# Kernel optimization log

Hardware: AMD Instinct MI355X
Metric: run time of the kernel (lower is better)

## Reference

```python
import jax, jax.numpy as jnp
import numpy as np

B, T, DIM, H, E, D, K = 2, 2048, 1024, 8, 5, 64, 3


def setup_inputs() -> dict:
    key = jax.random.key(0)
    ks = jax.random.split(key, 7)
    s = 0.02
    return {
        "x": jax.random.normal(ks[0], (B, T, DIM), dtype=jnp.float32),
        "w_q": jax.random.normal(ks[1], (DIM, H * E * D), dtype=jnp.float32) * s,
        "w_kv": jax.random.normal(ks[2], (DIM, 2 * H * E * D), dtype=jnp.float32) * s,
        "w_s": jax.random.normal(ks[3], (DIM, H * E), dtype=jnp.float32) * s,
        "w_d": jax.random.normal(ks[4], (DIM, H * E), dtype=jnp.float32) * s,
        "w_o_w": jax.random.normal(ks[5], (H, DIM, D), dtype=jnp.float32) * s,
        "w_o_b": jax.random.normal(ks[6], (H, DIM), dtype=jnp.float32) * s,
    }


def _select(proj_full, eps, s):
    # Faithful to torch scatter_(3, eps, s): value s[..., k] is written at
    # expert slot eps[..., k]; multiplying the full projection by that sparse
    # score tensor and summing over e == gather selected experts, weight by
    # the FIRST K raw scores (not the topk values), and sum.
    sel = jnp.take_along_axis(proj_full, eps[..., None], axis=3)  # b t h K d
    return (sel * s[..., :K, None]).sum(axis=3)  # b t h d


def reference(x, w_q, w_kv, w_s, w_d, w_o_w, w_o_b):
    scale = D ** (-0.5)
    ss = jax.nn.sigmoid(x @ w_s).reshape(B, T, H, E)
    sd = jax.nn.sigmoid(x @ w_d).reshape(B, T, H, E)
    eps_s = jax.lax.top_k(ss, K)[1]  # b t h K
    eps_d = jax.lax.top_k(sd, K)[1]

    q_full = (x @ w_q).reshape(B, T, H, E, D)
    q = _select(q_full, eps_d, sd)  # b t h d

    kv_full = (x @ w_kv).reshape(B, T, 2, H, E, D)
    k = _select(kv_full[:, :, 0], eps_s, ss)
    v = _select(kv_full[:, :, 1], eps_s, ss)

    attn = jnp.einsum("bihd,bjhd->bhij", q * scale, k)
    probs = jax.nn.softmax(attn, axis=-1)
    out = jnp.einsum("bhij,bjhd->bihd", probs, v)  # b t h d

    # per-head Linear(dim_head, dim) then sum over heads (stack+sum)
    return jnp.einsum("bihd,hfd->bif", out, w_o_w) + w_o_b.sum(axis=0)
```

## Files before the change

### kernel.cpp

```cpp
#include <hip/hip_runtime.h>

#define DEV __device__ __forceinline__

typedef float f32x4 __attribute__((ext_vector_type(4)));
typedef short s16x8 __attribute__((ext_vector_type(8)));
typedef unsigned short u16;
typedef unsigned int u32;

constexpr int Bb = 2, Tt = 2048, DIMc = 1024, Hh = 8, Ee = 5, Dd = 64;
constexpr int NTOK = Bb * Tt;
constexpr int NQ = Hh * Ee * Dd;

DEV u16 f2bf(float f) {
  union { float f; u32 u; } v; v.f = f;
  u32 r = v.u + 0x7fffu + ((v.u >> 16) & 1u);
  return (u16)(r >> 16);
}

DEV u32 pk2(float a, float b) {
  return (u32)f2bf(a) | ((u32)f2bf(b) << 16);
}

DEV s16x8 ld8(const u16* p) {
  uint4 u = *reinterpret_cast<const uint4*>(p);
  return __builtin_bit_cast(s16x8, u);
}

DEV f32x4 mfma16(s16x8 a, s16x8 b, f32x4 c) {
  return __builtin_amdgcn_mfma_f32_16x16x32_bf16(a, b, c, 0, 0, 0);
}

DEV void gld16(const void* g, void* l) {
  __builtin_amdgcn_global_load_lds(
      (const __attribute__((address_space(1))) void*)g,
      (__attribute__((address_space(3))) void*)l, 16, 0, 0);
}


__global__ void k_cvt_x(const float* __restrict__ x, u16* __restrict__ xb) {
  int i = blockIdx.x * blockDim.x + threadIdx.x;
  float4 v = reinterpret_cast<const float4*>(x)[i];
  u16 r0 = f2bf(v.x), r1 = f2bf(v.y), r2 = f2bf(v.z), r3 = f2bf(v.w);
  u32 lo = (u32)r0 | ((u32)r1 << 16);
  u32 hi = (u32)r2 | ((u32)r3 << 16);
  reinterpret_cast<uint2*>(xb)[i] = make_uint2(lo, hi);
}

__global__ void k_tr_w(const float* __restrict__ wq, const float* __restrict__ wkv,
                       u16* __restrict__ wT) {
  int R0 = blockIdx.x * 32;
  int C0 = blockIdx.y * 32;
  int s = R0 / 2560, rem = R0 % 2560;
  int h = rem / 320, n0 = rem % 320;
  const float* src; int ld; int col0;
  if (s == 0) { src = wq;  ld = 2560; col0 = h * 320 + n0; }
  else        { src = wkv; ld = 5120; col0 = (s - 1) * 2560 + h * 320 + n0; }
  __shared__ float tile[32][33];
  int tx = threadIdx.x, ty = threadIdx.y;
  #pragma unroll
  for (int i = 0; i < 4; i++) {
    int c = C0 + ty + 8 * i;
    tile[ty + 8 * i][tx] = src[(size_t)c * ld + col0 + tx];
  }
  __syncthreads();
  #pragma unroll
  for (int i = 0; i < 4; i++) {
    int n = ty + 8 * i;
    wT[(size_t)(R0 + n) * 1024 + C0 + tx] = f2bf(tile[tx][n]);
  }
}

__global__ void k_tr_wo(const float* __restrict__ wow, u16* __restrict__ woT) {
  int f = blockIdx.x, d = threadIdx.x;
  #pragma unroll
  for (int h = 0; h < 8; h++)
    woT[(size_t)f * 512 + h * 64 + d] = f2bf(wow[((size_t)h * 1024 + f) * 64 + d]);
}

__global__ void k_bias(const float* __restrict__ wob, float* __restrict__ biasum) {
  int f = blockIdx.x * 256 + threadIdx.x;
  float s = 0.f;
  #pragma unroll
  for (int h = 0; h < 8; h++) s += wob[h * 1024 + f];
  biasum[f] = s;
}

__global__ void k_tr_wsd(const float* __restrict__ ws, const float* __restrict__ wd,
                         float* __restrict__ wsdT) {
  int j = blockIdx.x;
  const float* src = (j < 40) ? ws : wd;
  int c = (j < 40) ? j : j - 40;
  for (int i = threadIdx.x; i < 1024; i += 256)
    wsdT[(size_t)j * 1024 + i] = src[(size_t)i * 40 + c];
}

__launch_bounds__(320)
__global__ void k_scores(const float* __restrict__ x, const float* __restrict__ wsdT,
                         int* __restrict__ eps_s, int* __restrict__ eps_d,
                         float* __restrict__ ss3, float* __restrict__ sd3) {
  int tokb = blockIdx.x * 8;
  __shared__ float xl[8][1028];
  __shared__ float sc[8][80];
  const float4* xsrc = reinterpret_cast<const float4*>(x + (size_t)tokb * 1024);
  for (int i = threadIdx.x; i < 2048; i += 320) {
    int tok = i >> 8, col4 = i & 255;
    *reinterpret_cast<float4*>(&xl[tok][col4 * 4]) = xsrc[i];
  }
  __syncthreads();
  {
    int tok = threadIdx.x & 7, j = threadIdx.x >> 3;
    const float4* wsp = reinterpret_cast<const float4*>(wsdT + (size_t)j * 1024);
    const float4* wdp = reinterpret_cast<const float4*>(wsdT + (size_t)(j + 40) * 1024);
    float as0 = 0.f, as1 = 0.f, ad0 = 0.f, ad1 = 0.f;
    #pragma unroll 4
    for (int k4 = 0; k4 < 256; k4 += 2) {
      float4 x0 = *reinterpret_cast<const float4*>(&xl[tok][k4 * 4]);
      float4 x1 = *reinterpret_cast<const float4*>(&xl[tok][k4 * 4 + 4]);
      float4 wsv0 = wsp[k4], wsv1 = wsp[k4 + 1];
      float4 wdv0 = wdp[k4], wdv1 = wdp[k4 + 1];
      as0 += x0.x * wsv0.x + x0.y * wsv0.y + x0.z * wsv0.z + x0.w * wsv0.w;
      as1 += x1.x * wsv1.x + x1.y * wsv1.y + x1.z * wsv1.z + x1.w * wsv1.w;
      ad0 += x0.x * wdv0.x + x0.y * wdv0.y + x0.z * wdv0.z + x0.w * wdv0.w;
      ad1 += x1.x * wdv1.x + x1.y * wdv1.y + x1.z * wdv1.z + x1.w * wdv1.w;
    }
    float as = as0 + as1, ad = ad0 + ad1;
    sc[tok][j]      = 1.f / (1.f + expf(-as));
    sc[tok][40 + j] = 1.f / (1.f + expf(-ad));
  }
  __syncthreads();
  int t2 = threadIdx.x;
  if (t2 < 128) {
    int tt = t2 >> 4, u = t2 & 15, h = u >> 1, which = u & 1;
    const float* S = &sc[tt][which * 40 + h * 5];
    float v[5];
    #pragma unroll
    for (int e = 0; e < 5; e++) v[e] = S[e];
    int tok = tokb + tt;
    int base = (tok * 8 + h) * 3;
    int* eps = which ? eps_d : eps_s;
    float* w3 = which ? sd3 : ss3;
    bool used[5] = {false, false, false, false, false};
    #pragma unroll
    for (int kk = 0; kk < 3; kk++) {
      float best = -1e30f; int bi = 0;
      #pragma unroll
      for (int e = 0; e < 5; e++)
        if (!used[e] && v[e] > best) { best = v[e]; bi = e; }
      used[bi] = true;
      eps[base + kk] = bi;
    }
    #pragma unroll
    for (int kk = 0; kk < 3; kk++) w3[base + kk] = S[kk];
  }
}

__launch_bounds__(512)
__global__ void k_proj(const u16* __restrict__ xb, const u16* __restrict__ wT,
                       const int* __restrict__ eps_d, const int* __restrict__ eps_s,
                       const float* __restrict__ sd3, const float* __restrict__ ss3,
                       u16* __restrict__ qw, u16* __restrict__ kw, u16* __restrict__ vw) {
  int tok0 = blockIdx.x * 128;
  int h = blockIdx.y;
  int s = blockIdx.z;
  int Rbase = (s * 8 + h) * 320;
  __shared__ alignas(16) u16 bsA[128 * 64];
  __shared__ alignas(16) u16 bsB[320 * 64];
  int wv = threadIdx.x >> 6, l = threadIdx.x & 63;
  int g = l >> 4, c = l & 15;
  f32x4 acc[20];
  #pragma unroll
  for (int i = 0; i < 20; i++) acc[i] = (f32x4){0.f, 0.f, 0.f, 0.f};

  const u16* wTp0 = wT + (size_t)Rbase * 1024;
  const u16* xbp0 = xb + (size_t)tok0 * 1024;

  for (int k0 = 0; k0 < 1024; k0 += 64) {
    __syncthreads();
    const u16* wTp = wTp0 + k0;
    #pragma unroll
    for (int j = 0; j < 5; j++) {
      int ch = wv * 320 + j * 64 + l;
      int row = ch >> 3, part = ch & 7;
      gld16(wTp + (size_t)row * 1024 + ((part * 8) ^ ((row & 7) * 8)),
            &bsB[(wv * 320 + j * 64) * 8]);
    }
    const u16* xbp = xbp0 + k0;
    #pragma unroll
    for (int j = 0; j < 2; j++) {
      int ch = wv * 128 + j * 64 + l;
      int row = ch >> 3, part = ch & 7;
      gld16(xbp + (size_t)row * 1024 + ((part * 8) ^ ((row & 7) * 8)),
            &bsA[(wv * 128 + j * 64) * 8]);
    }
    __syncthreads();

    #pragma unroll
    for (int kk = 0; kk < 2; kk++) {
      int off = (kk * 32 + g * 8) ^ ((c & 7) * 8);
      s16x8 a = *reinterpret_cast<const s16x8*>(&bsA[(wv * 16 + c) * 64 + off]);
      #pragma unroll
      for (int nt = 0; nt < 20; nt++) {
        s16x8 b = *reinterpret_cast<const s16x8*>(&bsB[(nt * 16 + c) * 64 + off]);
        acc[nt] = mfma16(a, b, acc[nt]);
      }
    }
  }

  const int* eps = (s == 0) ? eps_d : eps_s;
  const float* w3 = (s == 0) ? sd3 : ss3;
  float scale = (s == 0) ? 0.125f : 1.0f;
  u16* dst = (s == 0) ? qw : (s == 1 ? kw : vw);
  #pragma unroll
  for (int r = 0; r < 4; r++) {
    int tokr = tok0 + wv * 16 + g * 4 + r;
    int base = (tokr * 8 + h) * 3;
    int e0 = eps[base], e1 = eps[base + 1], e2 = eps[base + 2];
    float w0 = w3[base], w1 = w3[base + 1], w2 = w3[base + 2];
    float we[5];
    #pragma unroll
    for (int e = 0; e < 5; e++)
      we[e] = (e0 == e ? w0 : 0.f) + (e1 == e ? w1 : 0.f) + (e2 == e ? w2 : 0.f);
    int b = tokr >> 11, t = tokr & 2047;
    size_t obase = (((size_t)b * 8 + h) * 2048 + t) * 64;
    #pragma unroll
    for (int dh = 0; dh < 4; dh++) {
      float vq = 0.f;
      #pragma unroll
      for (int e = 0; e < 5; e++) vq += we[e] * acc[e * 4 + dh][r];
      dst[obase + dh * 16 + c] = f2bf(vq * scale);
    }
  }
}

__global__ void k_trv(const u16* __restrict__ vw, u16* __restrict__ vT) {
  int bh = blockIdx.z;
  int t0 = blockIdx.x * 32, d0 = blockIdx.y * 32;
  __shared__ u16 tile[32][33];
  const u16* src = vw + (size_t)bh * 2048 * 64;
  u16* dst = vT + (size_t)bh * 64 * 2048;
  int tx = threadIdx.x, ty = threadIdx.y;
  #pragma unroll
  for (int i = 0; i < 4; i++)
    tile[ty + 8 * i][tx] = src[(size_t)(t0 + ty + 8 * i) * 64 + d0 + tx];
  __syncthreads();
  int p = 8 * ((tx & 15) >> 2) + (tx & 3) + ((tx >= 16) ? 4 : 0);
  #pragma unroll
  for (int i = 0; i < 4; i++)
    dst[(size_t)(d0 + ty + 8 * i) * 2048 + t0 + p] = tile[tx][ty + 8 * i];
}

__launch_bounds__(256)
__global__ void k_attn(const u16* __restrict__ qw, const u16* __restrict__ kw,
                       const u16* __restrict__ vT, u16* __restrict__ ow) {
  int bh = blockIdx.y;
  int b = bh >> 3, h = bh & 7;
  int q0 = blockIdx.x * 64;
  int wv = threadIdx.x >> 6, l = threadIdx.x & 63;
  int g = l >> 4, c = l & 15;
  const u16* qp = qw + (size_t)bh * 2048 * 64;
  const u16* kp = kw + (size_t)bh * 2048 * 64;
  const u16* vp = vT + (size_t)bh * 64 * 2048;
  __shared__ alignas(16) u16 Kl[128 * 64];
  __shared__ alignas(16) u16 Vl[64 * 128];

  s16x8 qa0 = ld8(qp + (size_t)(q0 + wv * 16 + c) * 64 + 0 + 8 * g);
  s16x8 qa1 = ld8(qp + (size_t)(q0 + wv * 16 + c) * 64 + 32 + 8 * g);

  f32x4 o[4];
  #pragma unroll
  for (int i = 0; i < 4; i++) o[i] = (f32x4){0.f, 0.f, 0.f, 0.f};
  float ssum = 0.f;

  for (int kt = 0; kt < 2048; kt += 128) {
    __syncthreads();
    #pragma unroll
    for (int j = 0; j < 4; j++) {
      int ch = (wv * 4 + j) * 64 + l;
      int row = ch >> 3, sl = ch & 7;
      gld16(kp + (size_t)(kt + row) * 64 + ((sl ^ (row & 7)) * 8),
            &Kl[(wv * 4 + j) * 64 * 8]);
    }
    #pragma unroll
    for (int j = 0; j < 4; j++) {
      int ch = (wv * 4 + j) * 64 + l;
      int d = ch >> 4, sl = ch & 15;
      gld16(vp + (size_t)d * 2048 + kt + ((sl ^ (d & 15)) * 8),
            &Vl[(wv * 4 + j) * 64 * 8]);
    }
    __syncthreads();

    #pragma unroll
    for (int kk = 0; kk < 4; kk++) {
      int r0 = kk * 32 + c, r1 = kk * 32 + 16 + c;
      int c7 = c & 7;
      s16x8 ka0 = *reinterpret_cast<const s16x8*>(&Kl[r0 * 64 + ((0 + g) ^ c7) * 8]);
      s16x8 ka1 = *reinterpret_cast<const s16x8*>(&Kl[r0 * 64 + ((4 + g) ^ c7) * 8]);
      s16x8 kc0 = *reinterpret_cast<const s16x8*>(&Kl[r1 * 64 + ((0 + g) ^ c7) * 8]);
      s16x8 kc1 = *reinterpret_cast<const s16x8*>(&Kl[r1 * 64 + ((4 + g) ^ c7) * 8]);

      f32x4 s0 = (f32x4){0.f, 0.f, 0.f, 0.f};
      f32x4 s1 = (f32x4){0.f, 0.f, 0.f, 0.f};
      s0 = mfma16(ka0, qa0, s0);
      s0 = mfma16(ka1, qa1, s0);
      s1 = mfma16(kc0, qa0, s1);
      s1 = mfma16(kc1, qa1, s1);

      float p00 = __expf(s0[0]), p01 = __expf(s0[1]);
      float p02 = __expf(s0[2]), p03 = __expf(s0[3]);
      float p10 = __expf(s1[0]), p11 = __expf(s1[1]);
      float p12 = __expf(s1[2]), p13 = __expf(s1[3]);
      ssum += (p00 + p01) + (p02 + p03) + (p10 + p11) + (p12 + p13);

      uint4 pw = make_uint4(pk2(p00, p01), pk2(p02, p03),
                            pk2(p10, p11), pk2(p12, p13));
      s16x8 pa = __builtin_bit_cast(s16x8, pw);

      #pragma unroll
      for (int nt = 0; nt < 4; nt++) {
        int d = nt * 16 + c;
        s16x8 vb = *reinterpret_cast<const s16x8*>(&Vl[d * 128 + (((kk * 4 + g) ^ (d & 15)) * 8)]);
        o[nt] = mfma16(pa, vb, o[nt]);
      }
    }
  }

  ssum += __shfl_xor(ssum, 16, 64);
  ssum += __shfl_xor(ssum, 32, 64);
  #pragma unroll
  for (int r = 0; r < 4; r++) {
    float sm = __shfl(ssum, g * 4 + r, 64);
    float inv = 1.f / sm;
    int t = q0 + wv * 16 + g * 4 + r;
    #pragma unroll
    for (int nt = 0; nt < 4; nt++)
      ow[((size_t)(b * 2048 + t)) * 512 + h * 64 + nt * 16 + c] = f2bf(o[nt][r] * inv);
  }
}

__launch_bounds__(512)
__global__ void k_oproj(const u16* __restrict__ ow, const u16* __restrict__ woT,
                        const float* __restrict__ biasum, float* __restrict__ out) {
  int t0 = blockIdx.x * 128, f0 = blockIdx.y * 64;
  int wv = threadIdx.x >> 6, l = threadIdx.x & 63;
  int g = l >> 4, c = l & 15;
  f32x4 acc[4];
  #pragma unroll
  for (int i = 0; i < 4; i++) acc[i] = (f32x4){0.f, 0.f, 0.f, 0.f};
  for (int k0 = 0; k0 < 512; k0 += 32) {
    s16x8 a = ld8(ow + (size_t)(t0 + wv * 16 + c) * 512 + k0 + 8 * g);
    #pragma unroll
    for (int nt = 0; nt < 4; nt++) {
      s16x8 bfr = ld8(woT + (size_t)(f0 + nt * 16 + c) * 512 + k0 + 8 * g);
      acc[nt] = mfma16(a, bfr, acc[nt]);
    }
  }
  #pragma unroll
  for (int r = 0; r < 4; r++) {
    int t = t0 + wv * 16 + g * 4 + r;
    #pragma unroll
    for (int nt = 0; nt < 4; nt++) {
      int f = f0 + nt * 16 + c;
      out[(size_t)t * 1024 + f] = acc[nt][r] + biasum[f];
    }
  }
}

extern "C" void kernel_launch(void* const* d_in, const int* in_sizes, int n_in,
                              void* d_out, int out_size, void* d_ws, size_t ws_size,
                              hipStream_t stream) {
  const float* x    = (const float*)d_in[0];
  const float* w_q  = (const float*)d_in[1];
  const float* w_kv = (const float*)d_in[2];
  const float* w_s  = (const float*)d_in[3];
  const float* w_d  = (const float*)d_in[4];
  const float* w_ow = (const float*)d_in[5];
  const float* w_ob = (const float*)d_in[6];
  float* out = (float*)d_out;

  char* ws = (char*)d_ws;
  size_t o = 0;
  u16* xb     = (u16*)(ws + o); o += (size_t)NTOK * DIMc * 2;
  u16* wT     = (u16*)(ws + o); o += (size_t)3 * NQ * DIMc * 2;
  u16* woT    = (u16*)(ws + o); o += (size_t)1024 * 512 * 2;
  float* bsum = (float*)(ws + o); o += 4096;
  float* wsdT = (float*)(ws + o); o += (size_t)80 * 1024 * 4;
  int* eps_s  = (int*)(ws + o); o += (size_t)NTOK * 8 * 3 * 4;
  int* eps_d  = (int*)(ws + o); o += (size_t)NTOK * 8 * 3 * 4;
  float* ss3  = (float*)(ws + o); o += (size_t)NTOK * 8 * 3 * 4;
  float* sd3  = (float*)(ws + o); o += (size_t)NTOK * 8 * 3 * 4;
  u16* qw     = (u16*)(ws + o); o += (size_t)NTOK * 512 * 2;
  u16* kw     = (u16*)(ws + o); o += (size_t)NTOK * 512 * 2;
  u16* vw     = (u16*)(ws + o); o += (size_t)NTOK * 512 * 2;
  u16* vTw    = (u16*)(ws + o); o += (size_t)NTOK * 512 * 2;
  u16* oww    = (u16*)(ws + o); o += (size_t)NTOK * 512 * 2;

  k_cvt_x<<<4096, 256, 0, stream>>>(x, xb);
  k_tr_w<<<dim3(240, 32), dim3(32, 8), 0, stream>>>(w_q, w_kv, wT);
  k_tr_wo<<<1024, 64, 0, stream>>>(w_ow, woT);
  k_bias<<<4, 256, 0, stream>>>(w_ob, bsum);
  k_tr_wsd<<<80, 256, 0, stream>>>(w_s, w_d, wsdT);
  k_scores<<<512, 320, 0, stream>>>(x, wsdT, eps_s, eps_d, ss3, sd3);
  k_proj<<<dim3(32, 8, 3), 512, 0, stream>>>(xb, wT, eps_d, eps_s, sd3, ss3, qw, kw, vw);
  k_trv<<<dim3(64, 2, 16), dim3(32, 8), 0, stream>>>(vw, vTw);
  k_attn<<<dim3(32, 16), 256, 0, stream>>>(qw, kw, vTw, oww);
  k_oproj<<<dim3(32, 16), 512, 0, stream>>>(oww, woT, bsum, out);
}
```

Baseline: 225.3 us.

## Fuse prep kernels into one launch and shrink projection token tile

The five preprocessing kernels (x conversion, weight transposes, bias sum, score weight transpose) are merged into one kernel that dispatches on block index, removing four launches. The projection kernel now handles 64 tokens per block with 4 waves instead of 128 tokens with 8 waves. The A operand is loaded straight from global into registers rather than staged through LDS. This doubles the grid, frees the A tile's shared memory, and may improve occupancy. The cost is that each block re-reads the full 320-row weight tile for half as many tokens, doubling weight traffic, and the direct global A loads sit inside the k loop.

Result: no change. 227.9 us (+1.1%).

```diff
diff --git a/kernel.cpp b/kernel.cpp
--- a/kernel.cpp
+++ b/kernel.cpp
@@ -36,62 +36,63 @@
       (__attribute__((address_space(3))) void*)l, 16, 0, 0);
 }
 
-
-__global__ void k_cvt_x(const float* __restrict__ x, u16* __restrict__ xb) {
-  int i = blockIdx.x * blockDim.x + threadIdx.x;
-  float4 v = reinterpret_cast<const float4*>(x)[i];
-  u16 r0 = f2bf(v.x), r1 = f2bf(v.y), r2 = f2bf(v.z), r3 = f2bf(v.w);
-  u32 lo = (u32)r0 | ((u32)r1 << 16);
-  u32 hi = (u32)r2 | ((u32)r3 << 16);
-  reinterpret_cast<uint2*>(xb)[i] = make_uint2(lo, hi);
-}
-
-__global__ void k_tr_w(const float* __restrict__ wq, const float* __restrict__ wkv,
-                       u16* __restrict__ wT) {
-  int R0 = blockIdx.x * 32;
-  int C0 = blockIdx.y * 32;
-  int s = R0 / 2560, rem = R0 % 2560;
-  int h = rem / 320, n0 = rem % 320;
-  const float* src; int ld; int col0;
-  if (s == 0) { src = wq;  ld = 2560; col0 = h * 320 + n0; }
-  else        { src = wkv; ld = 5120; col0 = (s - 1) * 2560 + h * 320 + n0; }
-  __shared__ float tile[32][33];
-  int tx = threadIdx.x, ty = threadIdx.y;
-  #pragma unroll
-  for (int i = 0; i < 4; i++) {
-    int c = C0 + ty + 8 * i;
-    tile[ty + 8 * i][tx] = src[(size_t)c * ld + col0 + tx];
-  }
-  __syncthreads();
-  #pragma unroll
-  for (int i = 0; i < 4; i++) {
-    int n = ty + 8 * i;
-    wT[(size_t)(R0 + n) * 1024 + C0 + tx] = f2bf(tile[tx][n]);
-  }
-}
-
-__global__ void k_tr_wo(const float* __restrict__ wow, u16* __restrict__ woT) {
-  int f = blockIdx.x, d = threadIdx.x;
-  #pragma unroll
-  for (int h = 0; h < 8; h++)
-    woT[(size_t)f * 512 + h * 64 + d] = f2bf(wow[((size_t)h * 1024 + f) * 64 + d]);
-}
-
-__global__ void k_bias(const float* __restrict__ wob, float* __restrict__ biasum) {
-  int f = blockIdx.x * 256 + threadIdx.x;
-  float s = 0.f;
-  #pragma unroll
-  for (int h = 0; h < 8; h++) s += wob[h * 1024 + f];
-  biasum[f] = s;
-}
-
-__global__ void k_tr_wsd(const float* __restrict__ ws, const float* __restrict__ wd,
-                         float* __restrict__ wsdT) {
-  int j = blockIdx.x;
-  const float* src = (j < 40) ? ws : wd;
-  int c = (j < 40) ? j : j - 40;
-  for (int i = threadIdx.x; i < 1024; i += 256)
-    wsdT[(size_t)j * 1024 + i] = src[(size_t)i * 40 + c];
+__launch_bounds__(256)
+__global__ void k_prep(const float* __restrict__ x, const float* __restrict__ wq,
+                       const float* __restrict__ wkv, const float* __restrict__ wow,
+                       const float* __restrict__ wob, const float* __restrict__ wsr,
+                       const float* __restrict__ wdr,
+                       u16* __restrict__ xb, u16* __restrict__ wT,
+                       u16* __restrict__ woT, float* __restrict__ bsum,
+                       float* __restrict__ wsdT) {
+  int bid = blockIdx.x, t = threadIdx.x;
+  if (bid < 4096) {
+    int i = bid * 256 + t;
+    float4 v = reinterpret_cast<const float4*>(x)[i];
+    u16 r0 = f2bf(v.x), r1 = f2bf(v.y), r2 = f2bf(v.z), r3 = f2bf(v.w);
+    u32 lo = (u32)r0 | ((u32)r1 << 16);
+    u32 hi = (u32)r2 | ((u32)r3 << 16);
+    reinterpret_cast<uint2*>(xb)[i] = make_uint2(lo, hi);
+  } else if (bid < 11776) {
+    int b2 = bid - 4096;
+    int R0 = (b2 % 240) * 32;
+    int C0 = (b2 / 240) * 32;
+    int s = R0 / 2560, rem = R0 % 2560;
+    int h = rem / 320, n0 = rem % 320;
+    const float* src; int ld; int col0;
+    if (s == 0) { src = wq;  ld = 2560; col0 = h * 320 + n0; }
+    else        { src = wkv; ld = 5120; col0 = (s - 1) * 2560 + h * 320 + n0; }
+    __shared__ float tile[32][33];
+    int tx = t & 31, ty = t >> 5;
+    #pragma unroll
+    for (int i = 0; i < 4; i++) {
+      int c = C0 + ty + 8 * i;
+      tile[ty + 8 * i][tx] = src[(size_t)c * ld + col0 + tx];
+    }
+    __syncthreads();
+    #pragma unroll
+    for (int i = 0; i < 4; i++) {
+      int n = ty + 8 * i;
+      wT[(size_t)(R0 + n) * 1024 + C0 + tx] = f2bf(tile[tx][n]);
+    }
+  } else if (bid < 12032) {
+    int b2 = bid - 11776;
+    int f = b2 * 4 + (t >> 6), d = t & 63;
+    #pragma unroll
+    for (int h = 0; h < 8; h++)
+      woT[(size_t)f * 512 + h * 64 + d] = f2bf(wow[((size_t)h * 1024 + f) * 64 + d]);
+  } else if (bid < 12036) {
+    int f = (bid - 12032) * 256 + t;
+    float s = 0.f;
+    #pragma unroll
+    for (int h = 0; h < 8; h++) s += wob[h * 1024 + f];
+    bsum[f] = s;
+  } else {
+    int j = bid - 12036;
+    const float* src = (j < 40) ? wsr : wdr;
+    int c = (j < 40) ? j : j - 40;
+    for (int i = t; i < 1024; i += 256)
+      wsdT[(size_t)j * 1024 + i] = src[(size_t)i * 40 + c];
+  }
 }
 
 __launch_bounds__(320)
@@ -154,16 +155,15 @@
   }
 }
 
-__launch_bounds__(512)
+__launch_bounds__(256)
 __global__ void k_proj(const u16* __restrict__ xb, const u16* __restrict__ wT,
                        const int* __restrict__ eps_d, const int* __restrict__ eps_s,
                        const float* __restrict__ sd3, const float* __restrict__ ss3,
                        u16* __restrict__ qw, u16* __restrict__ kw, u16* __restrict__ vw) {
-  int tok0 = blockIdx.x * 128;
+  int tok0 = blockIdx.x * 64;
   int h = blockIdx.y;
   int s = blockIdx.z;
   int Rbase = (s * 8 + h) * 320;
-  __shared__ alignas(16) u16 bsA[128 * 64];
   __shared__ alignas(16) u16 bsB[320 * 64];
   int wv = threadIdx.x >> 6, l = threadIdx.x & 63;
   int g = l >> 4, c = l & 15;
@@ -172,36 +172,34 @@
   for (int i = 0; i < 20; i++) acc[i] = (f32x4){0.f, 0.f, 0.f, 0.f};
 
   const u16* wTp0 = wT + (size_t)Rbase * 1024;
-  const u16* xbp0 = xb + (size_t)tok0 * 1024;
+  const u16* xrow = xb + (size_t)(tok0 + wv * 16 + c) * 1024;
 
   for (int k0 = 0; k0 < 1024; k0 += 64) {
     __syncthreads();
     const u16* wTp = wTp0 + k0;
     #pragma unroll
-    for (int j = 0; j < 5; j++) {
-      int ch = wv * 320 + j * 64 + l;
+    for (int j = 0; j < 10; j++) {
+      int ch = wv * 640 + j * 64 + l;
       int row = ch >> 3, part = ch & 7;
       gld16(wTp + (size_t)row * 1024 + ((part * 8) ^ ((row & 7) * 8)),
-            &bsB[(wv * 320 + j * 64) * 8]);
-    }
-    const u16* xbp = xbp0 + k0;
-    #pragma unroll
-    for (int j = 0; j < 2; j++) {
-      int ch = wv * 128 + j * 64 + l;
-      int row = ch >> 3, part = ch & 7;
-      gld16(xbp + (size_t)row * 1024 + ((part * 8) ^ ((row & 7) * 8)),
-            &bsA[(wv * 128 + j * 64) * 8]);
-    }
+            &bsB[(wv * 640 + j * 64) * 8]);
+    }
+    s16x8 a0 = ld8(xrow + k0 + 8 * g);
+    s16x8 a1 = ld8(xrow + k0 + 32 + 8 * g);
     __syncthreads();
 
-    #pragma unroll
-    for (int kk = 0; kk < 2; kk++) {
-      int off = (kk * 32 + g * 8) ^ ((c & 7) * 8);
-      s16x8 a = *reinterpret_cast<const s16x8*>(&bsA[(wv * 16 + c) * 64 + off]);
+    {
+      int off0 = (g * 8) ^ ((c & 7) * 8);
       #pragma unroll
       for (int nt = 0; nt < 20; nt++) {
-        s16x8 b = *reinterpret_cast<const s16x8*>(&bsB[(nt * 16 + c) * 64 + off]);
-        acc[nt] = mfma16(a, b, acc[nt]);
+        s16x8 b = *reinterpret_cast<const s16x8*>(&bsB[(nt * 16 + c) * 64 + off0]);
+        acc[nt] = mfma16(a0, b, acc[nt]);
+      }
+      int off1 = (32 + g * 8) ^ ((c & 7) * 8);
+      #pragma unroll
+      for (int nt = 0; nt < 20; nt++) {
+        s16x8 b = *reinterpret_cast<const s16x8*>(&bsB[(nt * 16 + c) * 64 + off1]);
+        acc[nt] = mfma16(a1, b, acc[nt]);
       }
     }
   }
@@ -394,13 +392,10 @@
   u16* vTw    = (u16*)(ws + o); o += (size_t)NTOK * 512 * 2;
   u16* oww    = (u16*)(ws + o); o += (size_t)NTOK * 512 * 2;
 
-  k_cvt_x<<<4096, 256, 0, stream>>>(x, xb);
-  k_tr_w<<<dim3(240, 32), dim3(32, 8), 0, stream>>>(w_q, w_kv, wT);
-  k_tr_wo<<<1024, 64, 0, stream>>>(w_ow, woT);
-  k_bias<<<4, 256, 0, stream>>>(w_ob, bsum);
-  k_tr_wsd<<<80, 256, 0, stream>>>(w_s, w_d, wsdT);
+  k_prep<<<12116, 256, 0, stream>>>(x, w_q, w_kv, w_ow, w_ob, w_s, w_d,
+                                    xb, wT, woT, bsum, wsdT);
   k_scores<<<512, 320, 0, stream>>>(x, wsdT, eps_s, eps_d, ss3, sd3);
-  k_proj<<<dim3(32, 8, 3), 512, 0, stream>>>(xb, wT, eps_d, eps_s, sd3, ss3, qw, kw, vw);
+  k_proj<<<dim3(64, 8, 3), 256, 0, stream>>>(xb, wT, eps_d, eps_s, sd3, ss3, qw, kw, vw);
   k_trv<<<dim3(64, 2, 16), dim3(32, 8), 0, stream>>>(vw, vTw);
   k_attn<<<dim3(32, 16), 256, 0, stream>>>(qw, kw, vTw, oww);
   k_oproj<<<dim3(32, 16), 512, 0, stream>>>(oww, woT, bsum, out);
```
